# Optimization experiments

Hardware: AMD Instinct MI355X
Metric: run time of the kernel (lower is better)

Reference implementation:

```python
import jax, jax.numpy as jnp
import numpy as np

INPUT_CHANNELS = 3

def setup_inputs() -> dict:
    key = jax.random.key(0)
    kx, ky = jax.random.split(key)
    x = jax.random.normal(kx, (8, 4096, 3), dtype=jnp.float32)
    y = jax.random.normal(ky, (8, 4096, 3), dtype=jnp.float32)
    return {"x": x, "y": y}

def reference(x, y):
    # Match torch: truncate both clouds to common num_points and input_channels.
    num_points = min(x.shape[1], y.shape[1])
    x = x[:, :num_points, :INPUT_CHANNELS]
    y = y[:, :num_points, :INPUT_CHANNELS]
    # pdist[b, i, j] = ||x_i||^2 + ||y_j||^2 - 2 x_i . y_j  (squared Euclidean)
    x2 = jnp.sum(x * x, axis=-1)          # [B, N]
    y2 = jnp.sum(y * y, axis=-1)          # [B, N]
    zz = jnp.einsum('bic,bjc->bij', x, y) # [B, N, N]
    pdist = x2[:, :, None] + y2[:, None, :] - 2.0 * zz
    # min over i (dim 1): nearest x for each y; min over j (dim 2): nearest y for each x
    loss = jnp.mean(jnp.min(pdist, axis=1)) + jnp.mean(jnp.min(pdist, axis=2))
    return loss * 0.005
```

## Files before the change

### kernel.cpp

```cpp
#include <hip/hip_runtime.h>

#define NPTS 4096
#define NB   8

typedef __attribute__((ext_vector_type(8)))  short          bf16x8;
typedef __attribute__((ext_vector_type(8)))  unsigned short u16x8;
typedef __attribute__((ext_vector_type(16))) float          f32x16;

__device__ __forceinline__ unsigned short bf16_rne(float f) {
    unsigned u = __float_as_uint(f);
    u += 0x7FFFu + ((u >> 16) & 1u);
    return (unsigned short)(u >> 16);
}
__device__ __forceinline__ float bf16_f(unsigned short s) {
    return __uint_as_float(((unsigned)s) << 16);
}


__global__ __launch_bounds__(256, 1) void chamfer_fused(
    const float* __restrict__ x, const float* __restrict__ y,
    float* __restrict__ partials)
{
    extern __shared__ char smem[];
    unsigned short* sB = (unsigned short*)smem;
    float (*buf)[64][33] = (float (*)[64][33])smem;
    __shared__ float redb[4];

    const int bid  = blockIdx.x;
    const int dirb = bid >> 4;
    const int ib2  = bid & 15;

    const int tid = threadIdx.x;
    const int w   = tid >> 6;
    const int l   = tid & 63;
    const int g   = l >> 5;
    const int pos = l & 31;

    const float* Araw = (dirb < 8) ? x + (size_t)dirb * NPTS * 3
                                   : y + (size_t)(dirb - 8) * NPTS * 3;
    const int bcid = dirb ^ 8;
    const float* Braw = (bcid < 8) ? x + (size_t)bcid * NPTS * 3
                                   : y + (size_t)(bcid - 8) * NPTS * 3;

    #pragma unroll
    for (int k = 0; k < 16; ++k) {
        int p = k * 256 + tid;
        const float* src = Braw + (size_t)p * 3;
        float c0 = src[0], c1 = src[1], c2 = src[2];
        float h  = -0.5f * (c0 * c0 + c1 * c1 + c2 * c2);
        unsigned short h0 = bf16_rne(c0), h1 = bf16_rne(c1), h2 = bf16_rne(c2);
        unsigned short l0 = bf16_rne(c0 - bf16_f(h0));
        unsigned short l1 = bf16_rne(c1 - bf16_f(h1));
        unsigned short l2 = bf16_rne(c2 - bf16_f(h2));
        unsigned short hh = bf16_rne(h);
        unsigned short hl = bf16_rne(h - bf16_f(hh));
        u16x8 blo, bhi;
        blo[0]=h0; blo[1]=h1; blo[2]=h2; blo[3]=h0; blo[4]=h1; blo[5]=h2; blo[6]=l0; blo[7]=l1;
        bhi[0]=l2; bhi[1]=hh; bhi[2]=hl; bhi[3]=0; bhi[4]=0; bhi[5]=0; bhi[6]=0; bhi[7]=0;
        int u = p >> 5, ppos = p & 31;
        char* dst = (char*)sB + (size_t)u * 1024 + (size_t)ppos * 16;
        *(u16x8*)dst         = blo;
        *(u16x8*)(dst + 512) = bhi;
    }

    const int it0 = ib2 * 8 + w * 2;
    bf16x8 afr[2];
    #pragma unroll
    for (int t = 0; t < 2; ++t) {
        const float* ap = Araw + (size_t)((it0 + t) * 32 + pos) * 3;
        float c0 = ap[0], c1 = ap[1], c2 = ap[2];
        unsigned short h0 = bf16_rne(c0), h1 = bf16_rne(c1), h2 = bf16_rne(c2);
        unsigned short l0 = bf16_rne(c0 - bf16_f(h0));
        unsigned short l1 = bf16_rne(c1 - bf16_f(h1));
        unsigned short l2 = bf16_rne(c2 - bf16_f(h2));
        const short ONE = (short)0x3F80;
        bf16x8 alo, ahi;
        alo[0]=(short)h0; alo[1]=(short)h1; alo[2]=(short)h2; alo[3]=(short)l0;
        alo[4]=(short)l1; alo[5]=(short)l2; alo[6]=(short)h0; alo[7]=(short)h1;
        ahi[0]=(short)h2; ahi[1]=ONE; ahi[2]=ONE; ahi[3]=0;
        ahi[4]=0; ahi[5]=0; ahi[6]=0; ahi[7]=0;
        #pragma unroll
        for (int e = 0; e < 8; ++e) afr[t][e] = g ? ahi[e] : alo[e];
    }

    __syncthreads();

    f32x16 zc;
    #pragma unroll
    for (int r = 0; r < 16; ++r) zc[r] = 0.f;

    f32x16 run[2];
    #pragma unroll
    for (int t = 0; t < 2; ++t)
        #pragma unroll
        for (int r = 0; r < 16; ++r) run[t][r] = -3.0e38f;

    f32x16 p0, p1;
    #pragma unroll
    for (int r = 0; r < 16; ++r) { p0[r] = -3.0e38f; p1[r] = -3.0e38f; }

    const char* Bq = (const char*)sB + (size_t)g * 512 + (size_t)pos * 16;

    bf16x8 cb0 = *(const bf16x8*)(Bq);
    bf16x8 cb1 = *(const bf16x8*)(Bq + 1024);
    bf16x8 cb2 = *(const bf16x8*)(Bq + 2048);
    bf16x8 cb3 = *(const bf16x8*)(Bq + 3072);

#define STAGE(T, B0, B1, RP)                                                    \
    {                                                                           \
        f32x16 d0 = __builtin_amdgcn_mfma_f32_32x32x16_bf16(afr[T], B0, zc, 0, 0, 0); \
        f32x16 d1 = __builtin_amdgcn_mfma_f32_32x32x16_bf16(afr[T], B1, zc, 0, 0, 0); \
        _Pragma("unroll")                                                       \
        for (int r = 0; r < 16; ++r)                                            \
            run[RP][r] = fmaxf(fmaxf(p0[r], p1[r]), run[RP][r]);                \
        p0 = d0; p1 = d1;                                                       \
    }

    #pragma unroll 1
    for (int j = 0; j < 128; j += 4) {
        bf16x8 nb0, nb1, nb2, nb3;
        if (j < 124) {
            const char* Bn = Bq + (size_t)(j + 4) * 1024;
            nb0 = *(const bf16x8*)(Bn);
            nb1 = *(const bf16x8*)(Bn + 1024);
            nb2 = *(const bf16x8*)(Bn + 2048);
            nb3 = *(const bf16x8*)(Bn + 3072);
        }
        STAGE(0, cb0, cb1, 1)
        STAGE(1, cb0, cb1, 0)
        STAGE(0, cb2, cb3, 1)
        STAGE(1, cb2, cb3, 0)
        if (j < 124) { cb0 = nb0; cb1 = nb1; cb2 = nb2; cb3 = nb3; }
    }
#undef STAGE

    #pragma unroll
    for (int r = 0; r < 16; ++r)
        run[1][r] = fmaxf(fmaxf(p0[r], p1[r]), run[1][r]);

    __syncthreads();

    #pragma unroll
    for (int tl = 0; tl < 2; ++tl) {
        #pragma unroll
        for (int r = 0; r < 16; ++r) {
            int rowin = (r & 3) + 8 * (r >> 2) + 4 * g;
            buf[w][tl * 32 + rowin][pos] = run[tl][r];
        }
    }
    __syncthreads();

    float m = buf[w][l][0];
    #pragma unroll
    for (int k = 1; k < 32; ++k) m = fmaxf(m, buf[w][l][k]);

    int row = ib2 * 256 + w * 64 + l;
    const float* ap = Araw + (size_t)row * 3;
    float a0 = ap[0], a1 = ap[1], a2 = ap[2];
    float s = m - 0.5f * (a0 * a0 + a1 * a1 + a2 * a2);

    #pragma unroll
    for (int off = 32; off > 0; off >>= 1)
        s += __shfl_down(s, off);

    if (l == 0) redb[w] = s;
    __syncthreads();
    if (tid == 0)
        partials[bid] = redb[0] + redb[1] + redb[2] + redb[3];
}

__global__ __launch_bounds__(256) void final_reduce(
    const float* __restrict__ partials, float* __restrict__ out)
{
    float s = partials[threadIdx.x];
    #pragma unroll
    for (int off = 32; off > 0; off >>= 1)
        s += __shfl_down(s, off);

    __shared__ float redb[4];
    const int lane = threadIdx.x & 63, wave = threadIdx.x >> 6;
    if (lane == 0) redb[wave] = s;
    __syncthreads();
    if (threadIdx.x == 0) {
        out[0] = (redb[0] + redb[1] + redb[2] + redb[3])
                 * (-2.0f * 0.005f / 32768.f);
    }
}

extern "C" void kernel_launch(void* const* d_in, const int* in_sizes, int n_in,
                              void* d_out, int out_size, void* d_ws, size_t ws_size,
                              hipStream_t stream) {
    const float* x = (const float*)d_in[0];
    const float* y = (const float*)d_in[1];
    float* out = (float*)d_out;

    float* partials = (float*)d_ws;

    chamfer_fused<<<dim3(256), dim3(256), 131072, stream>>>(x, y, partials);
    final_reduce<<<dim3(1), dim3(256), 0, stream>>>(partials, out);
}
```

Before: 76.41 us.

## Split work into 512 blocks with half-size shared B staged in two passes

```diff
diff --git a/kernel.cpp b/kernel.cpp
--- a/kernel.cpp
+++ b/kernel.cpp
@@ -1,7 +1,6 @@
 #include <hip/hip_runtime.h>
 
 #define NPTS 4096
-#define NB   8
 
 typedef __attribute__((ext_vector_type(8)))  short          bf16x8;
 typedef __attribute__((ext_vector_type(8)))  unsigned short u16x8;
@@ -17,18 +16,18 @@
 }
 
 
-__global__ __launch_bounds__(256, 1) void chamfer_fused(
+__global__ __launch_bounds__(256, 2) void chamfer_fused(
     const float* __restrict__ x, const float* __restrict__ y,
     float* __restrict__ partials)
 {
     extern __shared__ char smem[];
     unsigned short* sB = (unsigned short*)smem;
-    float (*buf)[64][33] = (float (*)[64][33])smem;
+    float (*buf)[32][33] = (float (*)[32][33])smem;
     __shared__ float redb[4];
 
-    const int bid  = blockIdx.x;
-    const int dirb = bid >> 4;
-    const int ib2  = bid & 15;
+    const int bid   = blockIdx.x;
+    const int dirb  = bid >> 5;
+    const int islab = bid & 31;
 
     const int tid = threadIdx.x;
     const int w   = tid >> 6;
@@ -42,32 +41,10 @@
     const float* Braw = (bcid < 8) ? x + (size_t)bcid * NPTS * 3
                                    : y + (size_t)(bcid - 8) * NPTS * 3;
 
-    #pragma unroll
-    for (int k = 0; k < 16; ++k) {
-        int p = k * 256 + tid;
-        const float* src = Braw + (size_t)p * 3;
-        float c0 = src[0], c1 = src[1], c2 = src[2];
-        float h  = -0.5f * (c0 * c0 + c1 * c1 + c2 * c2);
-        unsigned short h0 = bf16_rne(c0), h1 = bf16_rne(c1), h2 = bf16_rne(c2);
-        unsigned short l0 = bf16_rne(c0 - bf16_f(h0));
-        unsigned short l1 = bf16_rne(c1 - bf16_f(h1));
-        unsigned short l2 = bf16_rne(c2 - bf16_f(h2));
-        unsigned short hh = bf16_rne(h);
-        unsigned short hl = bf16_rne(h - bf16_f(hh));
-        u16x8 blo, bhi;
-        blo[0]=h0; blo[1]=h1; blo[2]=h2; blo[3]=h0; blo[4]=h1; blo[5]=h2; blo[6]=l0; blo[7]=l1;
-        bhi[0]=l2; bhi[1]=hh; bhi[2]=hl; bhi[3]=0; bhi[4]=0; bhi[5]=0; bhi[6]=0; bhi[7]=0;
-        int u = p >> 5, ppos = p & 31;
-        char* dst = (char*)sB + (size_t)u * 1024 + (size_t)ppos * 16;
-        *(u16x8*)dst         = blo;
-        *(u16x8*)(dst + 512) = bhi;
-    }
-
-    const int it0 = ib2 * 8 + w * 2;
-    bf16x8 afr[2];
-    #pragma unroll
-    for (int t = 0; t < 2; ++t) {
-        const float* ap = Araw + (size_t)((it0 + t) * 32 + pos) * 3;
+    const int itile = islab * 4 + w;
+    bf16x8 afr;
+    {
+        const float* ap = Araw + (size_t)(itile * 32 + pos) * 3;
         float c0 = ap[0], c1 = ap[1], c2 = ap[2];
         unsigned short h0 = bf16_rne(c0), h1 = bf16_rne(c1), h2 = bf16_rne(c2);
         unsigned short l0 = bf16_rne(c0 - bf16_f(h0));
@@ -80,84 +57,103 @@
         ahi[0]=(short)h2; ahi[1]=ONE; ahi[2]=ONE; ahi[3]=0;
         ahi[4]=0; ahi[5]=0; ahi[6]=0; ahi[7]=0;
         #pragma unroll
-        for (int e = 0; e < 8; ++e) afr[t][e] = g ? ahi[e] : alo[e];
+        for (int e = 0; e < 8; ++e) afr[e] = g ? ahi[e] : alo[e];
     }
-
-    __syncthreads();
 
     f32x16 zc;
     #pragma unroll
     for (int r = 0; r < 16; ++r) zc[r] = 0.f;
 
-    f32x16 run[2];
+    f32x16 run, p0, p1;
     #pragma unroll
-    for (int t = 0; t < 2; ++t)
-        #pragma unroll
-        for (int r = 0; r < 16; ++r) run[t][r] = -3.0e38f;
+    for (int r = 0; r < 16; ++r) { run[r] = -3.0e38f; p0[r] = -3.0e38f; p1[r] = -3.0e38f; }
 
-    f32x16 p0, p1;
-    #pragma unroll
-    for (int r = 0; r < 16; ++r) { p0[r] = -3.0e38f; p1[r] = -3.0e38f; }
+    const char* BqBase = (const char*)sB + (size_t)g * 512 + (size_t)pos * 16;
 
-    const char* Bq = (const char*)sB + (size_t)g * 512 + (size_t)pos * 16;
-
-    bf16x8 cb0 = *(const bf16x8*)(Bq);
-    bf16x8 cb1 = *(const bf16x8*)(Bq + 1024);
-    bf16x8 cb2 = *(const bf16x8*)(Bq + 2048);
-    bf16x8 cb3 = *(const bf16x8*)(Bq + 3072);
-
-#define STAGE(T, B0, B1, RP)                                                    \
+#define STAGE(B0, B1)                                                           \
     {                                                                           \
-        f32x16 d0 = __builtin_amdgcn_mfma_f32_32x32x16_bf16(afr[T], B0, zc, 0, 0, 0); \
-        f32x16 d1 = __builtin_amdgcn_mfma_f32_32x32x16_bf16(afr[T], B1, zc, 0, 0, 0); \
+        f32x16 d0 = __builtin_amdgcn_mfma_f32_32x32x16_bf16(afr, B0, zc, 0, 0, 0); \
+        f32x16 d1 = __builtin_amdgcn_mfma_f32_32x32x16_bf16(afr, B1, zc, 0, 0, 0); \
         _Pragma("unroll")                                                       \
         for (int r = 0; r < 16; ++r)                                            \
-            run[RP][r] = fmaxf(fmaxf(p0[r], p1[r]), run[RP][r]);                \
+            run[r] = fmaxf(fmaxf(p0[r], p1[r]), run[r]);                        \
         p0 = d0; p1 = d1;                                                       \
     }
 
     #pragma unroll 1
-    for (int j = 0; j < 128; j += 4) {
-        bf16x8 nb0, nb1, nb2, nb3;
-        if (j < 124) {
-            const char* Bn = Bq + (size_t)(j + 4) * 1024;
-            nb0 = *(const bf16x8*)(Bn);
-            nb1 = *(const bf16x8*)(Bn + 1024);
-            nb2 = *(const bf16x8*)(Bn + 2048);
-            nb3 = *(const bf16x8*)(Bn + 3072);
+    for (int half = 0; half < 2; ++half) {
+        if (half) __syncthreads();
+
+        #pragma unroll
+        for (int k = 0; k < 8; ++k) {
+            int p = k * 256 + tid;
+            const float* src = Braw + (size_t)(half * 2048 + p) * 3;
+            float c0 = src[0], c1 = src[1], c2 = src[2];
+            float h  = -0.5f * (c0 * c0 + c1 * c1 + c2 * c2);
+            unsigned short h0 = bf16_rne(c0), h1 = bf16_rne(c1), h2 = bf16_rne(c2);
+            unsigned short l0 = bf16_rne(c0 - bf16_f(h0));
+            unsigned short l1 = bf16_rne(c1 - bf16_f(h1));
+            unsigned short l2 = bf16_rne(c2 - bf16_f(h2));
+            unsigned short hh = bf16_rne(h);
+            unsigned short hl = bf16_rne(h - bf16_f(hh));
+            u16x8 blo, bhi;
+            blo[0]=h0; blo[1]=h1; blo[2]=h2; blo[3]=h0; blo[4]=h1; blo[5]=h2; blo[6]=l0; blo[7]=l1;
+            bhi[0]=l2; bhi[1]=hh; bhi[2]=hl; bhi[3]=0; bhi[4]=0; bhi[5]=0; bhi[6]=0; bhi[7]=0;
+            int u = p >> 5, ppos = p & 31;
+            char* dst = (char*)sB + (size_t)u * 1024 + (size_t)ppos * 16;
+            *(u16x8*)dst         = blo;
+            *(u16x8*)(dst + 512) = bhi;
         }
-        STAGE(0, cb0, cb1, 1)
-        STAGE(1, cb0, cb1, 0)
-        STAGE(0, cb2, cb3, 1)
-        STAGE(1, cb2, cb3, 0)
-        if (j < 124) { cb0 = nb0; cb1 = nb1; cb2 = nb2; cb3 = nb3; }
+        __syncthreads();
+
+        bf16x8 cb0 = *(const bf16x8*)(BqBase);
+        bf16x8 cb1 = *(const bf16x8*)(BqBase + 1024);
+        bf16x8 cb2 = *(const bf16x8*)(BqBase + 2048);
+        bf16x8 cb3 = *(const bf16x8*)(BqBase + 3072);
+
+        #pragma unroll 1
+        for (int j = 0; j < 64; j += 4) {
+            bf16x8 nb0, nb1, nb2, nb3;
+            if (j < 60) {
+                const char* Bn = BqBase + (size_t)(j + 4) * 1024;
+                nb0 = *(const bf16x8*)(Bn);
+                nb1 = *(const bf16x8*)(Bn + 1024);
+                nb2 = *(const bf16x8*)(Bn + 2048);
+                nb3 = *(const bf16x8*)(Bn + 3072);
+            }
+            STAGE(cb0, cb1)
+            STAGE(cb2, cb3)
+            if (j < 60) { cb0 = nb0; cb1 = nb1; cb2 = nb2; cb3 = nb3; }
+        }
     }
 #undef STAGE
 
     #pragma unroll
     for (int r = 0; r < 16; ++r)
-        run[1][r] = fmaxf(fmaxf(p0[r], p1[r]), run[1][r]);
+        run[r] = fmaxf(fmaxf(p0[r], p1[r]), run[r]);
 
     __syncthreads();
 
     #pragma unroll
-    for (int tl = 0; tl < 2; ++tl) {
-        #pragma unroll
-        for (int r = 0; r < 16; ++r) {
-            int rowin = (r & 3) + 8 * (r >> 2) + 4 * g;
-            buf[w][tl * 32 + rowin][pos] = run[tl][r];
-        }
+    for (int r = 0; r < 16; ++r) {
+        int rowin = (r & 3) + 8 * (r >> 2) + 4 * g;
+        buf[w][rowin][pos] = run[r];
     }
     __syncthreads();
 
-    float m = buf[w][l][0];
+    float m = buf[w][l & 31][(l >> 5) * 16];
     #pragma unroll
-    for (int k = 1; k < 32; ++k) m = fmaxf(m, buf[w][l][k]);
+    for (int k = 1; k < 16; ++k)
+        m = fmaxf(m, buf[w][l & 31][(l >> 5) * 16 + k]);
+    m = fmaxf(m, __shfl_xor(m, 32));
 
-    int row = ib2 * 256 + w * 64 + l;
-    const float* ap = Araw + (size_t)row * 3;
-    float a0 = ap[0], a1 = ap[1], a2 = ap[2];
-    float s = m - 0.5f * (a0 * a0 + a1 * a1 + a2 * a2);
+    float s = 0.f;
+    if (l < 32) {
+        int row = itile * 32 + l;
+        const float* ap = Araw + (size_t)row * 3;
+        float a0 = ap[0], a1 = ap[1], a2 = ap[2];
+        s = m - 0.5f * (a0 * a0 + a1 * a1 + a2 * a2);
+    }
 
     #pragma unroll
     for (int off = 32; off > 0; off >>= 1)
@@ -172,7 +168,7 @@
 __global__ __launch_bounds__(256) void final_reduce(
     const float* __restrict__ partials, float* __restrict__ out)
 {
-    float s = partials[threadIdx.x];
+    float s = partials[threadIdx.x] + partials[threadIdx.x + 256];
     #pragma unroll
     for (int off = 32; off > 0; off >>= 1)
         s += __shfl_down(s, off);
@@ -196,6 +192,6 @@
 
     float* partials = (float*)d_ws;
 
-    chamfer_fused<<<dim3(256), dim3(256), 131072, stream>>>(x, y, partials);
+    chamfer_fused<<<dim3(512), dim3(256), 65536, stream>>>(x, y, partials);
     final_reduce<<<dim3(1), dim3(256), 0, stream>>>(partials, out);
 }
```

Result: faster. 70.19 us (-8.1%).
